# Performance work log

Measured on AMD Instinct MI355X. Metric: run time of the kernel, lower is better.

## Reference

```python
import jax, jax.numpy as jnp
import numpy as np

B, N, C, D, H, L, F = 64, 256, 16, 512, 8, 8, 2048
HD = D // H
PI = np.pi


def _ln(x, w, b, eps=1e-5):
    mu = jnp.mean(x, -1, keepdims=True)
    var = jnp.mean(jnp.square(x - mu), -1, keepdims=True)
    return (x - mu) * jax.lax.rsqrt(var + eps) * w + b


def _forward(x_node, x_full, Wp, bp, cls, e_w1, e_b1, e_w2, e_b2, edge_scale,
             qkv_w, qkv_b, out_w, out_b, ln1_w, ln1_b, ln2_w, ln2_b,
             ff1_w, ff1_b, ff2_w, ff2_b, cl_ln_w, cl_ln_b, cl_w1, cl_b1, cl_w2, cl_b2):
    Bq, Nq, _ = x_node.shape
    # pairwise kaon geometry from absolute y/phi
    y = x_full[:, :, 14]
    phi = x_full[:, :, 15]
    dy = jnp.abs(y[:, :, None] - y[:, None, :])                                  # [B,N,N]
    dphi = jnp.abs(jnp.mod(phi[:, :, None] - phi[:, None, :] + PI, 2 * PI) - PI)
    dr = jnp.sqrt(dy * dy + dphi * dphi + 1e-8)
    ef = jnp.stack([dy, dphi, dr], -1)                                           # [B,N,N,3]
    hmid = jax.nn.gelu(ef @ e_w1.T + e_b1, approximate=False)                    # [B,N,N,16]
    raw = hmid @ e_w2.T + e_b2                                                   # [B,N,N,H]
    central = jnp.mean(raw, axis=2).transpose(0, 2, 1)                           # [B,H,N]
    edge_bias = raw.transpose(0, 3, 1, 2)                                        # [B,H,N,N]
    bias = jnp.zeros((Bq, H, Nq + 1, Nq + 1), x_node.dtype)
    bias = bias.at[:, :, 1:, 1:].set(edge_bias)
    bias = bias.at[:, :, 0, 1:].set(central * edge_scale)
    bias = bias.at[:, :, 1:, 0].set(central * edge_scale)

    h = x_node @ Wp.T + bp
    h = jnp.concatenate([jnp.broadcast_to(cls, (Bq, 1, D)), h], axis=1)          # [B,S,D]
    S = Nq + 1
    scale = 1.0 / np.sqrt(HD)
    for l in range(L):  # pre-norm TransformerEncoderLayer (activation=relu, no final norm)
        x = _ln(h, ln1_w[l], ln1_b[l])
        qkv = x @ qkv_w[l].T + qkv_b[l]
        q, k, v = jnp.split(qkv, 3, axis=-1)
        q = q.reshape(Bq, S, H, HD).transpose(0, 2, 1, 3)
        k = k.reshape(Bq, S, H, HD).transpose(0, 2, 1, 3)
        v = v.reshape(Bq, S, H, HD).transpose(0, 2, 1, 3)
        scores = jnp.einsum('bhqd,bhkd->bhqk', q, k) * scale + bias
        attn = jax.nn.softmax(scores, axis=-1)
        o = jnp.einsum('bhqk,bhkd->bhqd', attn, v).transpose(0, 2, 1, 3).reshape(Bq, S, D)
        h = h + o @ out_w[l].T + out_b[l]
        x = _ln(h, ln2_w[l], ln2_b[l])
        h = h + jax.nn.relu(x @ ff1_w[l].T + ff1_b[l]) @ ff2_w[l].T + ff2_b[l]
    x = _ln(h[:, 0], cl_ln_w, cl_ln_b)
    return jax.nn.gelu(x @ cl_w1.T + cl_b1, approximate=False) @ cl_w2.T + cl_b2  # [B,2]


def setup_inputs() -> dict:
    key = jax.random.key(0)
    ks = iter(jax.random.split(key, 40))
    f32 = jnp.float32

    def nrm(shape, s=0.02):
        return (s * jax.random.normal(next(ks), shape)).astype(f32)

    return {
        'x_node': jax.random.normal(next(ks), (B, N, C), f32),
        'x_full': jax.random.normal(next(ks), (B, N, 16), f32),
        'Wp': nrm((D, C)), 'bp': jnp.zeros((D,), f32),
        'cls': nrm((1, 1, D)),
        'e_w1': nrm((16, 3), 0.3), 'e_b1': jnp.zeros((16,), f32),
        'e_w2': nrm((H, 16), 0.01), 'e_b2': jnp.zeros((H,), f32),
        'edge_scale': jnp.full((1,), 0.1, f32),
        'qkv_w': nrm((L, 3 * D, D)), 'qkv_b': jnp.zeros((L, 3 * D), f32),
        'out_w': nrm((L, D, D)), 'out_b': jnp.zeros((L, D), f32),
        'ln1_w': jnp.ones((L, D), f32), 'ln1_b': jnp.zeros((L, D), f32),
        'ln2_w': jnp.ones((L, D), f32), 'ln2_b': jnp.zeros((L, D), f32),
        'ff1_w': nrm((L, F, D)), 'ff1_b': jnp.zeros((L, F), f32),
        'ff2_w': nrm((L, D, F)), 'ff2_b': jnp.zeros((L, D), f32),
        'cl_ln_w': jnp.ones((D,), f32), 'cl_ln_b': jnp.zeros((D,), f32),
        'cl_w1': nrm((D // 2, D)), 'cl_b1': jnp.zeros((D // 2,), f32),
        'cl_w2': nrm((2, D // 2)), 'cl_b2': jnp.zeros((2,), f32),
    }


def reference(x_node, x_full, Wp, bp, cls, e_w1, e_b1, e_w2, e_b2, edge_scale,
              qkv_w, qkv_b, out_w, out_b, ln1_w, ln1_b, ln2_w, ln2_b,
              ff1_w, ff1_b, ff2_w, ff2_b, cl_ln_w, cl_ln_b, cl_w1, cl_b1, cl_w2, cl_b2):
    return _forward(x_node, x_full, Wp, bp, cls, e_w1, e_b1, e_w2, e_b2, edge_scale,
                    qkv_w, qkv_b, out_w, out_b, ln1_w, ln1_b, ln2_w, ln2_b,
                    ff1_w, ff1_b, ff2_w, ff2_b, cl_ln_w, cl_ln_b, cl_w1, cl_b1, cl_w2, cl_b2)
```

## Files before the change

### kernel.cpp

```cpp
#include <hip/hip_runtime.h>
#include <hip/hip_bf16.h>
#include <stdint.h>

#define PI_F     3.14159265358979323846f
#define TWO_PI_F 6.28318530717958647692f
#define INV2PI_F 0.15915494309189535f

typedef __attribute__((ext_vector_type(8))) short bf16x8;
typedef __attribute__((ext_vector_type(4))) float f32x4;

#define BB 64
#define NN 256
#define SS 257
#define DD 512
#define HH 8
#define HDD 64
#define LL 8
#define MTOK 16448
#define MPAD 16512
#define BSTR 264
#define VSTR 320

__device__ __forceinline__ float b2f(unsigned short u){
  union { float f; uint32_t i; } c; c.i = ((uint32_t)u) << 16; return c.f;
}
__device__ __forceinline__ unsigned short f2b(float f){
  union { float f; uint32_t i; } c; c.f = f;
  uint32_t r = c.i + 0x7FFFu + ((c.i >> 16) & 1u);
  return (unsigned short)(r >> 16);
}
__device__ __forceinline__ float gelu_fast(float z){
  const float z2 = z*z;
  const float u2 = z * (1.5957691216f + 0.071354816f*z2);
  const float e = __expf(u2);
  const float th = 1.f - 2.f/(1.f + e);
  return 0.5f*z*(1.f + th);
}

typedef __attribute__((address_space(1))) unsigned char ga_t;
typedef __attribute__((address_space(3))) unsigned char ls_t;
__device__ __forceinline__ void gl_lds16(const void* g, void* l){
  __builtin_amdgcn_global_load_lds((ga_t*)g, (ls_t*)l, 16, 0, 0);
}

__global__ __launch_bounds__(256) void cvt_kernel(const float* __restrict__ src,
                                                  unsigned short* __restrict__ dst, int n2){
  int i = blockIdx.x*256 + threadIdx.x;
  int stride = gridDim.x*256;
  for (; i < n2; i += stride){
    float2 v = ((const float2*)src)[i];
    ((uint32_t*)dst)[i] = (uint32_t)f2b(v.x) | ((uint32_t)f2b(v.y) << 16);
  }
}

__global__ __launch_bounds__(256) void edge_kernel(
    const float* __restrict__ x_full, const float* __restrict__ e_w1, const float* __restrict__ e_b1,
    const float* __restrict__ e_w2, const float* __restrict__ e_b2,
    unsigned short* __restrict__ bias, float* __restrict__ central)
{
  const int bi = blockIdx.x;
  const int b = bi >> 8, i = bi & 255;
  const int j = threadIdx.x;
  const float yi = x_full[((long)b*NN + i)*16 + 14];
  const float fi = x_full[((long)b*NN + i)*16 + 15];
  const float yj = x_full[((long)b*NN + j)*16 + 14];
  const float fj = x_full[((long)b*NN + j)*16 + 15];
  const float dy = fabsf(yi - yj);
  const float xw = fi - fj + PI_F;
  const float tw = xw * INV2PI_F;
  const float md = (tw - floorf(tw)) * TWO_PI_F;
  const float dphi = fabsf(md - PI_F);
  const float dr = sqrtf(dy*dy + dphi*dphi + 1e-8f);
  float raw[8];
  #pragma unroll
  for (int hh = 0; hh < 8; ++hh) raw[hh] = e_b2[hh];
  #pragma unroll
  for (int k = 0; k < 16; ++k){
    float z = e_w1[k*3]*dy + e_w1[k*3+1]*dphi + e_w1[k*3+2]*dr + e_b1[k];
    float g = gelu_fast(z);
    #pragma unroll
    for (int hh = 0; hh < 8; ++hh) raw[hh] += g * e_w2[hh*16 + k];
  }
  #pragma unroll
  for (int hh = 0; hh < 8; ++hh)
    bias[(((long)b*HH + hh)*SS + 1 + i)*BSTR + 1 + j] = f2b(raw[hh]);
  #pragma unroll
  for (int m = 1; m < 64; m <<= 1)
    #pragma unroll
    for (int hh = 0; hh < 8; ++hh) raw[hh] += __shfl_xor(raw[hh], m);
  __shared__ float cw[4][8];
  const int wv = j >> 6;
  if ((j & 63) == 0)
    for (int hh = 0; hh < 8; ++hh) cw[wv][hh] = raw[hh];
  __syncthreads();
  if (j < 8){
    float t = cw[0][j] + cw[1][j] + cw[2][j] + cw[3][j];
    central[((long)b*NN + i)*HH + j] = t * (1.f/NN);
  }
}

__global__ __launch_bounds__(256) void edge_border_kernel(
    const float* __restrict__ central, const float* __restrict__ edge_scale,
    unsigned short* __restrict__ bias)
{
  const int bh = blockIdx.x;
  const int b = bh >> 3, h = bh & 7;
  const int j = threadIdx.x;
  const float es = edge_scale[0];
  const float cv = central[((long)b*NN + j)*HH + h] * es;
  const long base = (long)bh*SS*BSTR;
  const unsigned short u = f2b(cv);
  bias[base + 1 + j] = u;
  bias[base + (long)(1+j)*BSTR] = u;
  if (j == 0) bias[base] = 0;
}

__global__ __launch_bounds__(256) void proj_kernel(
    const float* __restrict__ x_node, const float* __restrict__ Wp,
    const float* __restrict__ bp, const float* __restrict__ cls, float* __restrict__ hb)
{
  const int t = blockIdx.x;
  const int tid = threadIdx.x;
  const int b = t / SS, s2 = t - b*SS;
  float2 o;
  if (s2 == 0){
    o = *(const float2*)(cls + tid*2);
  } else {
    const float* xr = x_node + ((long)b*NN + (s2-1))*16;
    float xv[16];
    #pragma unroll
    for (int c2 = 0; c2 < 16; ++c2) xv[c2] = xr[c2];
    float oo[2];
    #pragma unroll
    for (int e = 0; e < 2; ++e){
      int d = tid*2 + e;
      float a = bp[d];
      const float* wr2 = Wp + (long)d*16;
      #pragma unroll
      for (int c2 = 0; c2 < 16; ++c2) a += xv[c2]*wr2[c2];
      oo[e] = a;
    }
    o.x = oo[0]; o.y = oo[1];
  }
  *(float2*)(hb + (long)t*DD + tid*2) = o;
}

__global__ __launch_bounds__(256) void ln_kernel(
    const float* __restrict__ hb, const float* __restrict__ w,
    const float* __restrict__ bbv, unsigned short* __restrict__ xb)
{
  const int tok = blockIdx.x*4 + (threadIdx.x >> 6);
  const int lane = threadIdx.x & 63;
  const float4* p = (const float4*)(hb + (long)tok*DD + lane*8);
  const float4 a = p[0], bq = p[1];
  float s  = a.x + a.y + a.z + a.w + bq.x + bq.y + bq.z + bq.w;
  float ss = a.x*a.x + a.y*a.y + a.z*a.z + a.w*a.w
           + bq.x*bq.x + bq.y*bq.y + bq.z*bq.z + bq.w*bq.w;
  #pragma unroll
  for (int m = 1; m < 64; m <<= 1){ s += __shfl_xor(s, m); ss += __shfl_xor(ss, m); }
  const float mu = s * (1.f/DD);
  const float var = ss * (1.f/DD) - mu*mu;
  const float rs = rsqrtf(var + 1e-5f);
  const float4* wp = (const float4*)(w + lane*8);
  const float4* bp2 = (const float4*)(bbv + lane*8);
  const float4 w0 = wp[0], w1 = wp[1];
  const float4 b0 = bp2[0], b1 = bp2[1];
  bf16x8 o;
  o[0] = (short)f2b((a.x - mu)*rs*w0.x + b0.x);
  o[1] = (short)f2b((a.y - mu)*rs*w0.y + b0.y);
  o[2] = (short)f2b((a.z - mu)*rs*w0.z + b0.z);
  o[3] = (short)f2b((a.w - mu)*rs*w0.w + b0.w);
  o[4] = (short)f2b((bq.x - mu)*rs*w1.x + b1.x);
  o[5] = (short)f2b((bq.y - mu)*rs*w1.y + b1.y);
  o[6] = (short)f2b((bq.z - mu)*rs*w1.z + b1.z);
  o[7] = (short)f2b((bq.w - mu)*rs*w1.w + b1.w);
  *(bf16x8*)(xb + (long)tok*DD + lane*8) = o;
}

template<int EPI, int NI>
__global__ __launch_bounds__(256, 4) void gemm_kernel(
    const unsigned short* __restrict__ A, const unsigned short* __restrict__ Bw,
    const float* __restrict__ bias, void* __restrict__ Cout,
    int M, int N, int K, int ldc, int nblocks)
{
  __shared__ unsigned short As[128*64];
  __shared__ unsigned short Bs[NI*32*64];
  const int tid = threadIdx.x;
  const int lane = tid & 63;
  const int wave = tid >> 6;
  const int wr = wave >> 1, wc = wave & 1;
  const int l16 = lane & 15, lhi = lane >> 4;

  const int nwg = gridDim.x;
  const int q8 = nwg >> 3, r8 = nwg & 7;
  const int xcd = blockIdx.x & 7, idx = blockIdx.x >> 3;
  const int lin = (xcd < r8 ? xcd*(q8+1) : r8*(q8+1) + (xcd-r8)*q8) + idx;
  const int mb = lin / nblocks;
  const int nb = lin - mb*nblocks;
  const long m0 = (long)mb * 128;
  const long n0 = (long)nb * (NI*32);

  f32x4 acc[4][NI];
  const f32x4 z4 = {0.f, 0.f, 0.f, 0.f};
  #pragma unroll
  for (int mi = 0; mi < 4; ++mi)
    #pragma unroll
    for (int ni = 0; ni < NI; ++ni) acc[mi][ni] = z4;

  const char* Ab = (const char*)A;
  const char* Bb = (const char*)Bw;
  const int nkt = K >> 6;
  for (int kt = 0; kt < nkt; ++kt){
    #pragma unroll
    for (int c = 0; c < 4; ++c){
      const int bo = c*4096 + tid*16;
      const int row = bo >> 7;
      const int kb = bo & 127;
      gl_lds16(Ab + ((m0+row)*(long)K)*2 + (long)kt*128 + kb, (char*)As + bo);
    }
    #pragma unroll
    for (int c = 0; c < NI; ++c){
      const int bo = c*4096 + tid*16;
      const int row = bo >> 7;
      const int kb = bo & 127;
      gl_lds16(Bb + ((n0+row)*(long)K)*2 + (long)kt*128 + kb, (char*)Bs + bo);
    }
    __syncthreads();
    #pragma unroll
    for (int kd = 0; kd < 2; ++kd){
      bf16x8 af[4], bfr[NI];
      #pragma unroll
      for (int mi = 0; mi < 4; ++mi)
        af[mi] = *(const bf16x8*)((const char*)As + (wr*64 + mi*16 + l16)*128 + kd*64 + lhi*16);
      #pragma unroll
      for (int ni = 0; ni < NI; ++ni)
        bfr[ni] = *(const bf16x8*)((const char*)Bs + (wc*(NI*16) + ni*16 + l16)*128 + kd*64 + lhi*16);
      #pragma unroll
      for (int mi = 0; mi < 4; ++mi)
        #pragma unroll
        for (int ni = 0; ni < NI; ++ni)
          acc[mi][ni] = __builtin_amdgcn_mfma_f32_16x16x32_bf16(af[mi], bfr[ni], acc[mi][ni], 0, 0, 0);
    }
    __syncthreads();
  }
  #pragma unroll
  for (int mi = 0; mi < 4; ++mi){
    #pragma unroll
    for (int ni = 0; ni < NI; ++ni){
      const int col = (int)n0 + wc*(NI*16) + ni*16 + l16;
      const float bn = bias[col];
      const int rowb = (int)m0 + wr*64 + mi*16 + lhi*4;
      #pragma unroll
      for (int r = 0; r < 4; ++r){
        const int m = rowb + r;
        if (m < M){
          float v = acc[mi][ni][r] + bn;
          if (EPI == 1) v = fmaxf(v, 0.f);
          if (EPI == 2) ((float*)Cout)[(long)m*ldc + col] += v;
          else          ((unsigned short*)Cout)[(long)m*ldc + col] = f2b(v);
        }
      }
    }
  }
}

__global__ __launch_bounds__(256) void vtrans_kernel(
    const unsigned short* __restrict__ qkv, unsigned short* __restrict__ vt)
{
  const int bh = blockIdx.x;
  const int c = blockIdx.y;
  const int b = bh >> 3, h = bh & 7;
  __shared__ unsigned short tile[64][72];
  const int tid = threadIdx.x;
  const int rr = tid >> 3, ch = tid & 7;
  #pragma unroll
  for (int it = 0; it < 2; ++it){
    const int sl = it*32 + rr;
    const long tok = (long)b*SS + c*64 + sl;
    bf16x8 v = *(const bf16x8*)(qkv + tok*1536 + 1024 + h*64 + ch*8);
    *(bf16x8*)(&tile[sl][ch*8]) = v;
  }
  __syncthreads();
  #pragma unroll
  for (int it = 0; it < 2; ++it){
    const int d = it*32 + rr;
    const int s0 = c*64 + ch*8;
    bf16x8 o;
    #pragma unroll
    for (int e = 0; e < 8; ++e){
      const int sgl = s0 + e;
      o[e] = (sgl < SS) ? (short)tile[ch*8 + e][d] : (short)0;
    }
    *(bf16x8*)(vt + ((long)bh*HDD + d)*VSTR + s0) = o;
  }
}

__global__ __launch_bounds__(576) void flash_kernel(
    const unsigned short* __restrict__ qkv, const unsigned short* __restrict__ vt,
    const unsigned short* __restrict__ bias, unsigned short* __restrict__ ob)
{
  const int bh = blockIdx.x;
  const int b = bh >> 3, h = bh & 7;
  const int qt = threadIdx.x >> 6;
  const int lane = threadIdx.x & 63;
  const int l16 = lane & 15, lhi = lane >> 4;

  __shared__ unsigned short Ks[2][2048];
  __shared__ unsigned short Vs[2][2048];
  __shared__ unsigned short Bsh[9][2][1024];
  __shared__ unsigned short pt[9][1024];
  unsigned short* ptw = pt[qt];

  bf16x8 qf[2][2];
  #pragma unroll
  for (int mi = 0; mi < 2; ++mi)
    #pragma unroll
    for (int kd = 0; kd < 2; ++kd){
      const long tok = (long)b*SS + qt*32 + mi*16 + l16;
      qf[mi][kd] = *(const bf16x8*)(qkv + tok*1536 + h*64 + kd*32 + lhi*8);
    }

  auto stage = [&](int jtn, int bb){
    const int rB = lane >> 2, cB = lane & 3;
    const char* gb = (const char*)bias + (((long)bh*SS + qt*32)*BSTR + (long)jtn*32)*2;
    char* lb = (char*)&Bsh[qt][bb][0];
    gl_lds16(gb + (long)rB*BSTR*2        + cB*16, lb + lane*16);
    gl_lds16(gb + (long)(16+rB)*BSTR*2   + cB*16, lb + 1024 + lane*16);
    if (qt < 4){
      const int rK = lane >> 3, cK = lane & 7;
      gl_lds16((const char*)qkv + (((long)b*SS + jtn*32 + qt*8 + rK)*1536 + 512 + h*64)*2 + ((cK ^ rK)*16),
               (char*)&Ks[bb][0] + qt*1024 + lane*16);
    } else if (qt < 8){
      const int rV = lane >> 2, cV = lane & 3;
      const int d = (qt-4)*16 + rV;
      gl_lds16((const char*)vt + (((long)bh*64 + d)*VSTR + (long)jtn*32)*2 + ((cV ^ (rV & 3))*16),
               (char*)&Vs[bb][0] + (qt-4)*1024 + lane*16);
    }
  };

  f32x4 oacc[2][4];
  const f32x4 z4 = {0.f, 0.f, 0.f, 0.f};
  #pragma unroll
  for (int mi = 0; mi < 2; ++mi)
    #pragma unroll
    for (int ni = 0; ni < 4; ++ni) oacc[mi][ni] = z4;
  float mrow[2][4], lrow[2][4];
  #pragma unroll
  for (int mi = 0; mi < 2; ++mi)
    #pragma unroll
    for (int r = 0; r < 4; ++r){ mrow[mi][r] = -1e30f; lrow[mi][r] = 0.f; }

  stage(0, 0);
  __builtin_amdgcn_sched_barrier(0);

  for (int jt = 0; jt < 9; ++jt){
    const int cur = jt & 1;
    if (jt < 8){
      stage(jt+1, cur ^ 1);
      __builtin_amdgcn_sched_barrier(0);
      if (qt < 8) asm volatile("s_waitcnt vmcnt(3)" ::: "memory");
      else        asm volatile("s_waitcnt vmcnt(2)" ::: "memory");
    } else {
      asm volatile("s_waitcnt vmcnt(0)" ::: "memory");
    }
    __builtin_amdgcn_sched_barrier(0);
    __builtin_amdgcn_s_barrier();
    __builtin_amdgcn_sched_barrier(0);

    bf16x8 kf[2][2];
    #pragma unroll
    for (int ni = 0; ni < 2; ++ni)
      #pragma unroll
      for (int kd = 0; kd < 2; ++kd){
        const int row = ni*16 + l16;
        const int sw = (kd*4 + lhi) ^ (row & 7);
        kf[ni][kd] = *(const bf16x8*)((const char*)&Ks[cur][0] + row*128 + sw*16);
      }
    f32x4 sacc[2][2];
    #pragma unroll
    for (int mi = 0; mi < 2; ++mi)
      #pragma unroll
      for (int ni = 0; ni < 2; ++ni) sacc[mi][ni] = z4;
    __builtin_amdgcn_s_setprio(1);
    #pragma unroll
    for (int kd = 0; kd < 2; ++kd)
      #pragma unroll
      for (int mi = 0; mi < 2; ++mi)
        #pragma unroll
        for (int ni = 0; ni < 2; ++ni)
          sacc[mi][ni] = __builtin_amdgcn_mfma_f32_16x16x32_bf16(qf[mi][kd], kf[ni][kd], sacc[mi][ni], 0, 0, 0);
    __builtin_amdgcn_s_setprio(0);

    float sv[2][2][4];
    #pragma unroll
    for (int mi = 0; mi < 2; ++mi)
      #pragma unroll
      for (int ni = 0; ni < 2; ++ni)
        #pragma unroll
        for (int r = 0; r < 4; ++r){
          const int col = jt*32 + ni*16 + l16;
          float x = sacc[mi][ni][r] * 0.125f;
          x += b2f(Bsh[qt][cur][(mi*16 + lhi*4 + r)*32 + ni*16 + l16]);
          if (col >= SS) x = -1e30f;
          sv[mi][ni][r] = x;
        }
    #pragma unroll
    for (int mi = 0; mi < 2; ++mi)
      #pragma unroll
      for (int r = 0; r < 4; ++r){
        float pm = fmaxf(sv[mi][0][r], sv[mi][1][r]);
        #pragma unroll
        for (int sh = 1; sh < 16; sh <<= 1) pm = fmaxf(pm, __shfl_xor(pm, sh));
        const float mold = mrow[mi][r];
        const float mnew = fmaxf(mold, pm);
        const float corr = __expf(mold - mnew);
        mrow[mi][r] = mnew;
        float psum = 0.f;
        #pragma unroll
        for (int ni = 0; ni < 2; ++ni){
          const float p = __expf(sv[mi][ni][r] - mnew);
          sv[mi][ni][r] = p;
          psum += p;
        }
        #pragma unroll
        for (int sh = 1; sh < 16; sh <<= 1) psum += __shfl_xor(psum, sh);
        lrow[mi][r] = lrow[mi][r]*corr + psum;
        #pragma unroll
        for (int ni = 0; ni < 4; ++ni) oacc[mi][ni][r] = oacc[mi][ni][r]*corr;
      }
    #pragma unroll
    for (int mi = 0; mi < 2; ++mi)
      #pragma unroll
      for (int ni = 0; ni < 2; ++ni)
        #pragma unroll
        for (int r = 0; r < 4; ++r)
          ptw[(mi*16 + lhi*4 + r)*32 + ni*16 + l16] = f2b(sv[mi][ni][r]);
    bf16x8 pf[2];
    #pragma unroll
    for (int mi = 0; mi < 2; ++mi)
      pf[mi] = *(const bf16x8*)(ptw + (mi*16 + l16)*32 + lhi*8);
    bf16x8 vf[4];
    #pragma unroll
    for (int ni = 0; ni < 4; ++ni){
      const int d = ni*16 + l16;
      const int sw = lhi ^ (d & 3);
      vf[ni] = *(const bf16x8*)((const char*)&Vs[cur][0] + d*64 + sw*16);
    }
    __builtin_amdgcn_s_setprio(1);
    #pragma unroll
    for (int mi = 0; mi < 2; ++mi)
      #pragma unroll
      for (int ni = 0; ni < 4; ++ni)
        oacc[mi][ni] = __builtin_amdgcn_mfma_f32_16x16x32_bf16(pf[mi], vf[ni], oacc[mi][ni], 0, 0, 0);
    __builtin_amdgcn_s_setprio(0);

    __builtin_amdgcn_sched_barrier(0);
    __builtin_amdgcn_s_barrier();
    __builtin_amdgcn_sched_barrier(0);
  }

  #pragma unroll
  for (int mi = 0; mi < 2; ++mi)
    #pragma unroll
    for (int r = 0; r < 4; ++r){
      const int row = qt*32 + mi*16 + lhi*4 + r;
      if (row < SS){
        const float inv = 1.0f / lrow[mi][r];
        const long tok = (long)b*SS + row;
        #pragma unroll
        for (int ni = 0; ni < 4; ++ni)
          ob[tok*DD + h*HDD + ni*16 + l16] = f2b(oacc[mi][ni][r] * inv);
      }
    }
}

__global__ __launch_bounds__(256) void cls_kernel(
    const float* __restrict__ hb, const float* __restrict__ lw, const float* __restrict__ lb,
    const float* __restrict__ w1, const float* __restrict__ b1,
    const float* __restrict__ w2, const float* __restrict__ b2, float* __restrict__ out)
{
  const int b = blockIdx.x;
  const int tid = threadIdx.x;
  const float* row = hb + (long)b*SS*DD;
  const float2 v = *(const float2*)(row + tid*2);
  float s = v.x + v.y, ss = v.x*v.x + v.y*v.y;
  #pragma unroll
  for (int m = 1; m < 64; m <<= 1){ s += __shfl_xor(s, m); ss += __shfl_xor(ss, m); }
  __shared__ float red[8];
  const int wv = tid >> 6;
  if ((tid & 63) == 0){ red[wv] = s; red[4+wv] = ss; }
  __syncthreads();
  s  = red[0]+red[1]+red[2]+red[3];
  ss = red[4]+red[5]+red[6]+red[7];
  const float mu = s * (1.f/DD);
  const float var = ss * (1.f/DD) - mu*mu;
  const float rs = rsqrtf(var + 1e-5f);
  __shared__ __align__(16) float xs[DD];
  xs[tid*2]   = (v.x - mu)*rs*lw[tid*2]   + lb[tid*2];
  xs[tid*2+1] = (v.y - mu)*rs*lw[tid*2+1] + lb[tid*2+1];
  __syncthreads();
  float a = b1[tid];
  const float4* w1v = (const float4*)(w1 + (long)tid*DD);
  const float4* xsv = (const float4*)xs;
  for (int d4 = 0; d4 < DD/4; ++d4){
    const float4 wv4 = w1v[d4], xv4 = xsv[d4];
    a += wv4.x*xv4.x + wv4.y*xv4.y + wv4.z*xv4.z + wv4.w*xv4.w;
  }
  const float g = 0.5f*a*(1.f + erff(a*0.70710678118f));
  float p0 = g * w2[tid];
  float p1 = g * w2[256 + tid];
  #pragma unroll
  for (int m = 1; m < 64; m <<= 1){ p0 += __shfl_xor(p0, m); p1 += __shfl_xor(p1, m); }
  __shared__ float r2[8];
  if ((tid & 63) == 0){ r2[wv] = p0; r2[4+wv] = p1; }
  __syncthreads();
  if (tid == 0) out[b*2]   = r2[0]+r2[1]+r2[2]+r2[3] + b2[0];
  if (tid == 1) out[b*2+1] = r2[4]+r2[5]+r2[6]+r2[7] + b2[1];
}

extern "C" void kernel_launch(void* const* d_in, const int* in_sizes, int n_in,
                              void* d_out, int out_size, void* d_ws, size_t ws_size,
                              hipStream_t stream) {
  const float* x_node    = (const float*)d_in[0];
  const float* x_full    = (const float*)d_in[1];
  const float* Wp        = (const float*)d_in[2];
  const float* bp        = (const float*)d_in[3];
  const float* cls       = (const float*)d_in[4];
  const float* e_w1      = (const float*)d_in[5];
  const float* e_b1      = (const float*)d_in[6];
  const float* e_w2      = (const float*)d_in[7];
  const float* e_b2      = (const float*)d_in[8];
  const float* edge_scale= (const float*)d_in[9];
  const float* qkv_w     = (const float*)d_in[10];
  const float* qkv_b     = (const float*)d_in[11];
  const float* out_w     = (const float*)d_in[12];
  const float* out_b     = (const float*)d_in[13];
  const float* ln1_w     = (const float*)d_in[14];
  const float* ln1_b     = (const float*)d_in[15];
  const float* ln2_w     = (const float*)d_in[16];
  const float* ln2_b     = (const float*)d_in[17];
  const float* ff1_w     = (const float*)d_in[18];
  const float* ff1_b     = (const float*)d_in[19];
  const float* ff2_w     = (const float*)d_in[20];
  const float* ff2_b     = (const float*)d_in[21];
  const float* cl_ln_w   = (const float*)d_in[22];
  const float* cl_ln_b   = (const float*)d_in[23];
  const float* cl_w1     = (const float*)d_in[24];
  const float* cl_b1     = (const float*)d_in[25];
  const float* cl_w2     = (const float*)d_in[26];
  const float* cl_b2     = (const float*)d_in[27];
  float* out = (float*)d_out;

  char* w = (char*)d_ws;
  size_t off = 0;
  auto take = [&](size_t bytes)->char*{
    char* p = w + off;
    off += (bytes + 255) & ~(size_t)255;
    return p;
  };
  unsigned short* wq8   = (unsigned short*)take((size_t)LL*1536*512*2);
  unsigned short* wo8   = (unsigned short*)take((size_t)LL*512*512*2);
  unsigned short* wf1   = (unsigned short*)take((size_t)LL*2048*512*2);
  unsigned short* wf2   = (unsigned short*)take((size_t)LL*512*2048*2);
  unsigned short* bias16= (unsigned short*)take((size_t)BB*HH*SS*BSTR*2 + 65536);
  float*          cent  = (float*)take((size_t)BB*NN*HH*4);
  float*          hbuf  = (float*)take((size_t)MPAD*DD*4);
  unsigned short* xb    = (unsigned short*)take((size_t)MPAD*DD*2);
  unsigned short* obuf  = (unsigned short*)take((size_t)MPAD*DD*2);
  unsigned short* qkvb  = (unsigned short*)take((size_t)MPAD*1536*2);
  unsigned short* vtb   = (unsigned short*)take((size_t)BB*HH*HDD*VSTR*2);
  unsigned short* ffb   = qkvb;

  cvt_kernel<<<4096, 256, 0, stream>>>(qkv_w, wq8, LL*1536*512/2);
  cvt_kernel<<<4096, 256, 0, stream>>>(out_w, wo8, LL*512*512/2);
  cvt_kernel<<<4096, 256, 0, stream>>>(ff1_w, wf1, LL*2048*512/2);
  cvt_kernel<<<4096, 256, 0, stream>>>(ff2_w, wf2, LL*512*2048/2);

  edge_kernel<<<dim3(BB*NN), 256, 0, stream>>>(x_full, e_w1, e_b1, e_w2, e_b2, bias16, cent);
  edge_border_kernel<<<dim3(BB*HH), 256, 0, stream>>>(cent, edge_scale, bias16);
  proj_kernel<<<dim3(MTOK), 256, 0, stream>>>(x_node, Wp, bp, cls, hbuf);

  for (int l = 0; l < LL; ++l){
    ln_kernel<<<dim3(MTOK/4), 256, 0, stream>>>(hbuf, ln1_w + l*DD, ln1_b + l*DD, xb);
    gemm_kernel<0,4><<<dim3(129*12), 256, 0, stream>>>(xb, wq8 + (size_t)l*1536*512,
        qkv_b + (size_t)l*1536, qkvb, MTOK, 1536, 512, 1536, 12);
    vtrans_kernel<<<dim3(512, 5), 256, 0, stream>>>(qkvb, vtb);
    flash_kernel<<<dim3(512), 576, 0, stream>>>(qkvb, vtb, bias16, obuf);
    gemm_kernel<2,2><<<dim3(129*8), 256, 0, stream>>>(obuf, wo8 + (size_t)l*512*512,
        out_b + (size_t)l*DD, hbuf, MTOK, 512, 512, 512, 8);
    ln_kernel<<<dim3(MTOK/4), 256, 0, stream>>>(hbuf, ln2_w + l*DD, ln2_b + l*DD, xb);
    gemm_kernel<1,4><<<dim3(129*16), 256, 0, stream>>>(xb, wf1 + (size_t)l*2048*512,
        ff1_b + (size_t)l*2048, ffb, MTOK, 2048, 512, 2048, 16);
    gemm_kernel<2,2><<<dim3(129*8), 256, 0, stream>>>(ffb, wf2 + (size_t)l*512*2048,
        ff2_b + (size_t)l*DD, hbuf, MTOK, 512, 2048, 512, 8);
  }
  cls_kernel<<<dim3(BB), 256, 0, stream>>>(hbuf, cl_ln_w, cl_ln_b, cl_w1, cl_b1, cl_w2, cl_b2, out);
}
```

Baseline: 2.619 ms.

## Double-buffer LDS tiles in NI=2 GEMMs to overlap loads with MFMA

Adds a PIPE template parameter to the GEMM. When it is set, the kernel uses two LDS buffers and prefetches the next K tile into one while MFMAs run on the other, with one barrier per iteration instead of two. MFMA sections are also wrapped in s_setprio to raise wave priority. The pipelined variant is used for the out-projection and FF2 GEMMs. It doubles their LDS use and lowers launch bounds occupancy from 4 to 3 blocks, trading latency hiding for fewer resident waves.

```diff
diff --git a/kernel.cpp b/kernel.cpp
--- a/kernel.cpp
+++ b/kernel.cpp
@@ -177,14 +177,14 @@
   *(bf16x8*)(xb + (long)tok*DD + lane*8) = o;
 }
 
-template<int EPI, int NI>
-__global__ __launch_bounds__(256, 4) void gemm_kernel(
+template<int EPI, int NI, int PIPE>
+__global__ __launch_bounds__(256, PIPE ? 3 : 4) void gemm_kernel(
     const unsigned short* __restrict__ A, const unsigned short* __restrict__ Bw,
     const float* __restrict__ bias, void* __restrict__ Cout,
     int M, int N, int K, int ldc, int nblocks)
 {
-  __shared__ unsigned short As[128*64];
-  __shared__ unsigned short Bs[NI*32*64];
+  __shared__ unsigned short As[(PIPE+1)*128*64];
+  __shared__ unsigned short Bs[(PIPE+1)*NI*32*64];
   const int tid = threadIdx.x;
   const int lane = tid & 63;
   const int wave = tid >> 6;
@@ -210,39 +210,66 @@
   const char* Ab = (const char*)A;
   const char* Bb = (const char*)Bw;
   const int nkt = K >> 6;
-  for (int kt = 0; kt < nkt; ++kt){
+
+  auto stage = [&](int kt, int sb){
     #pragma unroll
     for (int c = 0; c < 4; ++c){
       const int bo = c*4096 + tid*16;
       const int row = bo >> 7;
       const int kb = bo & 127;
-      gl_lds16(Ab + ((m0+row)*(long)K)*2 + (long)kt*128 + kb, (char*)As + bo);
+      gl_lds16(Ab + ((m0+row)*(long)K)*2 + (long)kt*128 + kb, (char*)As + sb*16384 + bo);
     }
     #pragma unroll
     for (int c = 0; c < NI; ++c){
       const int bo = c*4096 + tid*16;
       const int row = bo >> 7;
       const int kb = bo & 127;
-      gl_lds16(Bb + ((n0+row)*(long)K)*2 + (long)kt*128 + kb, (char*)Bs + bo);
-    }
-    __syncthreads();
+      gl_lds16(Bb + ((n0+row)*(long)K)*2 + (long)kt*128 + kb, (char*)Bs + sb*NI*4096 + bo);
+    }
+  };
+  auto compute = [&](int sb){
     #pragma unroll
     for (int kd = 0; kd < 2; ++kd){
       bf16x8 af[4], bfr[NI];
       #pragma unroll
       for (int mi = 0; mi < 4; ++mi)
-        af[mi] = *(const bf16x8*)((const char*)As + (wr*64 + mi*16 + l16)*128 + kd*64 + lhi*16);
+        af[mi] = *(const bf16x8*)((const char*)As + sb*16384 + (wr*64 + mi*16 + l16)*128 + kd*64 + lhi*16);
       #pragma unroll
       for (int ni = 0; ni < NI; ++ni)
-        bfr[ni] = *(const bf16x8*)((const char*)Bs + (wc*(NI*16) + ni*16 + l16)*128 + kd*64 + lhi*16);
+        bfr[ni] = *(const bf16x8*)((const char*)Bs + sb*NI*4096 + (wc*(NI*16) + ni*16 + l16)*128 + kd*64 + lhi*16);
+      __builtin_amdgcn_s_setprio(1);
       #pragma unroll
       for (int mi = 0; mi < 4; ++mi)
         #pragma unroll
         for (int ni = 0; ni < NI; ++ni)
           acc[mi][ni] = __builtin_amdgcn_mfma_f32_16x16x32_bf16(af[mi], bfr[ni], acc[mi][ni], 0, 0, 0);
-    }
-    __syncthreads();
-  }
+      __builtin_amdgcn_s_setprio(0);
+    }
+  };
+
+  if (PIPE == 0){
+    for (int kt = 0; kt < nkt; ++kt){
+      stage(kt, 0);
+      __syncthreads();
+      compute(0);
+      __syncthreads();
+    }
+  } else {
+    stage(0, 0);
+    asm volatile("s_waitcnt vmcnt(0)" ::: "memory");
+    __builtin_amdgcn_s_barrier();
+    int bb = 0;
+    for (int kt = 0; kt < nkt; ++kt){
+      if (kt + 1 < nkt) stage(kt + 1, bb ^ 1);
+      compute(bb);
+      if (kt + 1 < nkt){
+        asm volatile("s_waitcnt vmcnt(0)" ::: "memory");
+        __builtin_amdgcn_s_barrier();
+      }
+      bb ^= 1;
+    }
+  }
+
   #pragma unroll
   for (int mi = 0; mi < 4; ++mi){
     #pragma unroll
@@ -582,16 +609,16 @@
 
   for (int l = 0; l < LL; ++l){
     ln_kernel<<<dim3(MTOK/4), 256, 0, stream>>>(hbuf, ln1_w + l*DD, ln1_b + l*DD, xb);
-    gemm_kernel<0,4><<<dim3(129*12), 256, 0, stream>>>(xb, wq8 + (size_t)l*1536*512,
+    gemm_kernel<0,4,0><<<dim3(129*12), 256, 0, stream>>>(xb, wq8 + (size_t)l*1536*512,
         qkv_b + (size_t)l*1536, qkvb, MTOK, 1536, 512, 1536, 12);
     vtrans_kernel<<<dim3(512, 5), 256, 0, stream>>>(qkvb, vtb);
     flash_kernel<<<dim3(512), 576, 0, stream>>>(qkvb, vtb, bias16, obuf);
-    gemm_kernel<2,2><<<dim3(129*8), 256, 0, stream>>>(obuf, wo8 + (size_t)l*512*512,
+    gemm_kernel<2,2,1><<<dim3(129*8), 256, 0, stream>>>(obuf, wo8 + (size_t)l*512*512,
         out_b + (size_t)l*DD, hbuf, MTOK, 512, 512, 512, 8);
     ln_kernel<<<dim3(MTOK/4), 256, 0, stream>>>(hbuf, ln2_w + l*DD, ln2_b + l*DD, xb);
-    gemm_kernel<1,4><<<dim3(129*16), 256, 0, stream>>>(xb, wf1 + (size_t)l*2048*512,
+    gemm_kernel<1,4,0><<<dim3(129*16), 256, 0, stream>>>(xb, wf1 + (size_t)l*2048*512,
         ff1_b + (size_t)l*2048, ffb, MTOK, 2048, 512, 2048, 16);
-    gemm_kernel<2,2><<<dim3(129*8), 256, 0, stream>>>(ffb, wf2 + (size_t)l*512*2048,
+    gemm_kernel<2,2,1><<<dim3(129*8), 256, 0, stream>>>(ffb, wf2 + (size_t)l*512*2048,
         ff2_b + (size_t)l*DD, hbuf, MTOK, 512, 2048, 512, 8);
   }
   cls_kernel<<<dim3(BB), 256, 0, stream>>>(hbuf, cl_ln_w, cl_ln_b, cl_w1, cl_b1, cl_w2, cl_b2, out);
```

Result: slower. 2.791 ms (+6.6%).
